# Optimization experiments

Measured on AMD Instinct MI355X. Metric: run time of the kernel, lower is better.

Reference implementation:

```python
import jax, jax.numpy as jnp
import numpy as np

B, S, D, MAX_LEN = 8, 2048, 512, 2048
NEG_INF = jnp.float32(-jnp.inf)


def setup_inputs() -> dict:
    key = jax.random.key(0)
    ks = jax.random.split(key, 10)
    s = 1.0 / np.sqrt(D)
    inp = {
        "x": jax.random.normal(ks[0], (B, S, D), dtype=jnp.float32),
        "pos_table": jax.random.normal(ks[1], (MAX_LEN, D), dtype=jnp.float32) * 0.02,
        "Wq": jax.random.normal(ks[2], (D, D), dtype=jnp.float32) * s,
        "bq": jnp.zeros((D,), dtype=jnp.float32),
        "Wk": jax.random.normal(ks[3], (D, D), dtype=jnp.float32) * s,
        "bk": jnp.zeros((D,), dtype=jnp.float32),
        "Wv": jax.random.normal(ks[4], (D, D), dtype=jnp.float32) * s,
        "bv": jnp.zeros((D,), dtype=jnp.float32),
        "Wd": jax.random.normal(ks[5], (D, D), dtype=jnp.float32) * s,
        "bd": jnp.zeros((D,), dtype=jnp.float32),
    }
    return inp


def reference(x, pos_table, Wq, bq, Wk, bk, Wv, bv, Wd, bd):
    # add learned positional embeddings (add_pos=True path): arange over seq dim
    x = x + pos_table[:x.shape[-2]]  # [B,S,D]
    # torch nn.Linear: y = x @ W.T + b
    q = jnp.einsum("bsd,ed->bse", x, Wq) + bq
    k = jnp.einsum("bsd,ed->bse", x, Wk) + bk
    v = jnp.einsum("bsd,ed->bse", x, Wv) + bv
    v = jnp.where(jnp.isnan(v), 0.0, v)  # nan_to_num(nan=0)
    scale = 1.0 / jnp.sqrt(jnp.float32(D))
    scores = jnp.einsum("bqd,bkd->bqk", q, k) * scale  # [B,S,S]
    scores = jnp.where(jnp.isnan(scores), NEG_INF, scores)  # nan_to_num(nan=-inf)
    attn = jax.nn.softmax(scores, axis=2)
    y = jnp.einsum("bqk,bkd->bqd", attn, v)
    return jnp.einsum("bsd,ed->bse", y, Wd) + bd
```

## Files before the change

### kernel.cpp

```cpp
#include <hip/hip_runtime.h>
#include <stdint.h>

typedef __bf16 bf16x8 __attribute__((ext_vector_type(8)));
typedef float f32x4 __attribute__((ext_vector_type(4)));

static constexpr float QK_SCALE = 0.044194173824159216f;

__device__ __forceinline__ uint16_t f2bf(float f) {
    uint32_t x = __builtin_bit_cast(uint32_t, f);
    x += 0x7FFFu + ((x >> 16) & 1u);
    return (uint16_t)(x >> 16);
}

__device__ __forceinline__ void cp16(const uint16_t* g, uint16_t* l) {
    __builtin_amdgcn_global_load_lds(
        (__attribute__((address_space(1))) void*)(uint16_t*)g,
        (__attribute__((address_space(3))) void*)l,
        16, 0, 0);
}

template <int MODE>
__global__ __launch_bounds__(256, 2) void gemm_nt(
    const uint16_t* __restrict__ A, const uint16_t* __restrict__ Bm,
    void* __restrict__ C0, void* __restrict__ C1, void* __restrict__ C2,
    const float* __restrict__ bias0, const float* __restrict__ bias1,
    const float* __restrict__ bias2,
    float scale, int K, int ldc, long bsA, long bsB, long bsC)
{
    __shared__ __align__(16) uint16_t SH[4][8192];

    const int t  = threadIdx.x;
    const int bn = blockIdx.x, bm = blockIdx.y, bz = blockIdx.z;
    const int wave = t >> 6, lane = t & 63;
    const int wm = (wave >> 1) * 64, wn = (wave & 1) * 64;
    const int lm = lane & 15, lq = lane >> 4;
    const int sw = lq ^ ((lm >> 1) & 3);

    const uint16_t* Ab = A  + (long)bz * bsA + (long)bm * 128 * K;
    const uint16_t* Bb = Bm + (long)bz * bsB + (long)bn * 128 * K;

    long goff[2]; int loff[2];
#pragma unroll
    for (int j = 0; j < 2; ++j) {
        const int s  = j * 256 + t;
        const int r  = s >> 2;
        const int cs = s & 3;
        const int cg = cs ^ ((r >> 1) & 3);
        goff[j] = (long)r * K + cg * 8;
        loff[j] = s * 8;
    }

    const int KI = K >> 5;

#pragma unroll
    for (int st = 0; st < 3; ++st)
#pragma unroll
        for (int j = 0; j < 2; ++j) {
            cp16(Ab + goff[j] + st * 32, SH[st] + loff[j]);
            cp16(Bb + goff[j] + st * 32, SH[st] + 4096 + loff[j]);
        }

    f32x4 acc[4][4] = {};

    for (int k = 0; k < KI; ++k) {
        asm volatile("s_waitcnt vmcnt(8) lgkmcnt(0)\n\ts_barrier" ::: "memory");

        int kp = k + 3; if (kp >= KI) kp -= KI;
        uint16_t* dst = SH[(k + 3) & 3];
        const long ko = (long)kp * 32;
#pragma unroll
        for (int j = 0; j < 2; ++j) {
            cp16(Ab + goff[j] + ko, dst + loff[j]);
            cp16(Bb + goff[j] + ko, dst + 4096 + loff[j]);
        }

        const uint16_t* buf = SH[k & 3];
        bf16x8 af[4], bfr[4];
#pragma unroll
        for (int i = 0; i < 4; ++i)
            af[i]  = *(const bf16x8*)&buf[((wm + i * 16 + lm) * 4 + sw) * 8];
#pragma unroll
        for (int i = 0; i < 4; ++i)
            bfr[i] = *(const bf16x8*)&buf[4096 + ((wn + i * 16 + lm) * 4 + sw) * 8];
#pragma unroll
        for (int i = 0; i < 4; ++i)
#pragma unroll
            for (int j = 0; j < 4; ++j)
                acc[i][j] = __builtin_amdgcn_mfma_f32_16x16x32_bf16(
                    bfr[i], af[j], acc[i][j], 0, 0, 0);
    }

    const int mb = bm * 128 + wm + lm;
    const int nb = bn * 128 + wn + lq * 4;
#pragma unroll
    for (int i = 0; i < 4; ++i) {
        const int n = nb + i * 16;
        if (MODE == 0) {
#pragma unroll
            for (int j = 0; j < 4; ++j) {
                const int m = mb + j * 16;
                const uint32_t lo = (uint32_t)f2bf(acc[i][j][0] * scale) |
                                    ((uint32_t)f2bf(acc[i][j][1] * scale) << 16);
                const uint32_t hi = (uint32_t)f2bf(acc[i][j][2] * scale) |
                                    ((uint32_t)f2bf(acc[i][j][3] * scale) << 16);
                *(uint2*)&((uint16_t*)C0)[(long)bz * bsC + (long)m * ldc + n] =
                    make_uint2(lo, hi);
            }
        } else if (MODE == 2) {
            const float4 b4 = *(const float4*)&bias0[n];
#pragma unroll
            for (int j = 0; j < 4; ++j) {
                const int m = mb + j * 16;
                *(float4*)&((float*)C0)[(long)m * ldc + n] = make_float4(
                    acc[i][j][0] + b4.x, acc[i][j][1] + b4.y,
                    acc[i][j][2] + b4.z, acc[i][j][3] + b4.w);
            }
        } else {
            const int sec = n >> 9, nn = n & 511;
            const float* bp = sec == 0 ? bias0 : (sec == 1 ? bias1 : bias2);
            const float4 b4 = *(const float4*)&bp[nn];
#pragma unroll
            for (int j = 0; j < 4; ++j) {
                const int m = mb + j * 16;
                if (sec < 2) {
                    uint16_t* Cq = (uint16_t*)(sec == 0 ? C0 : C1);
                    const uint32_t lo = (uint32_t)f2bf(acc[i][j][0] + b4.x) |
                                        ((uint32_t)f2bf(acc[i][j][1] + b4.y) << 16);
                    const uint32_t hi = (uint32_t)f2bf(acc[i][j][2] + b4.z) |
                                        ((uint32_t)f2bf(acc[i][j][3] + b4.w) << 16);
                    *(uint2*)&Cq[(long)m * 512 + nn] = make_uint2(lo, hi);
                } else {
                    const int bb = m >> 11, ss = m & 2047;
                    uint16_t* vt = (uint16_t*)C2 + ((long)bb * 512 + nn) * 2048 + ss;
                    vt[0]        = f2bf(acc[i][j][0] + b4.x);
                    vt[2048]     = f2bf(acc[i][j][1] + b4.y);
                    vt[2 * 2048] = f2bf(acc[i][j][2] + b4.z);
                    vt[3 * 2048] = f2bf(acc[i][j][3] + b4.w);
                }
            }
        }
    }
}

__global__ __launch_bounds__(256) void prep_x(const float* __restrict__ x,
                                              const float* __restrict__ pos,
                                              uint16_t* __restrict__ xb)
{
    const long i8 = ((long)blockIdx.x * 256 + threadIdx.x) * 8;
    const long p8 = i8 & ((1l << 20) - 1);
    const float4* xv = (const float4*)(x + i8);
    const float4* pv = (const float4*)(pos + p8);
    const float4 a0 = xv[0], a1 = xv[1];
    const float4 b0 = pv[0], b1 = pv[1];
    uint16_t o[8];
    o[0] = f2bf(a0.x + b0.x); o[1] = f2bf(a0.y + b0.y);
    o[2] = f2bf(a0.z + b0.z); o[3] = f2bf(a0.w + b0.w);
    o[4] = f2bf(a1.x + b1.x); o[5] = f2bf(a1.y + b1.y);
    o[6] = f2bf(a1.z + b1.z); o[7] = f2bf(a1.w + b1.w);
    *(uint4*)(xb + i8) = *(uint4*)o;
}

__global__ __launch_bounds__(256) void prep_w(
    const float* __restrict__ Wq, const float* __restrict__ Wk,
    const float* __restrict__ Wv, const float* __restrict__ Wd,
    uint16_t* __restrict__ wqkv, uint16_t* __restrict__ wd)
{
    const long f = ((long)blockIdx.x * 256 + threadIdx.x) * 8;
    const int  w = (int)(f >> 18);
    const long off = f & 262143;
    const float* src = (w == 0) ? Wq : (w == 1) ? Wk : (w == 2) ? Wv : Wd;
    uint16_t* dst = (w < 3) ? (wqkv + (long)w * 262144 + off) : (wd + off);
    const float4* s4 = (const float4*)(src + off);
    const float4 a = s4[0], b = s4[1];
    uint16_t o[8];
    o[0] = f2bf(a.x); o[1] = f2bf(a.y); o[2] = f2bf(a.z); o[3] = f2bf(a.w);
    o[4] = f2bf(b.x); o[5] = f2bf(b.y); o[6] = f2bf(b.z); o[7] = f2bf(b.w);
    *(uint4*)dst = *(uint4*)o;
}

__global__ __launch_bounds__(256) void softmax_rows(uint16_t* __restrict__ P)
{
    uint16_t* p = P + (long)blockIdx.x * 2048;
    const int t = threadIdx.x;
    const int lane = t & 63, wave = t >> 6;

    uint4 raw = *(const uint4*)(p + t * 8);
    uint32_t u[4] = {raw.x, raw.y, raw.z, raw.w};
    float x[8];
#pragma unroll
    for (int i = 0; i < 4; ++i) {
        x[2 * i]     = __builtin_bit_cast(float, u[i] << 16);
        x[2 * i + 1] = __builtin_bit_cast(float, u[i] & 0xFFFF0000u);
    }
    float mx = x[0];
#pragma unroll
    for (int i = 1; i < 8; ++i) mx = fmaxf(mx, x[i]);
#pragma unroll
    for (int off = 32; off; off >>= 1) mx = fmaxf(mx, __shfl_xor(mx, off));
    __shared__ float sm[4], ss[4];
    if (lane == 0) sm[wave] = mx;
    __syncthreads();
    mx = fmaxf(fmaxf(sm[0], sm[1]), fmaxf(sm[2], sm[3]));

    float sum = 0.f;
#pragma unroll
    for (int i = 0; i < 8; ++i) { x[i] = __expf(x[i] - mx); sum += x[i]; }
#pragma unroll
    for (int off = 32; off; off >>= 1) sum += __shfl_xor(sum, off);
    if (lane == 0) ss[wave] = sum;
    __syncthreads();
    const float inv = 1.f / (ss[0] + ss[1] + ss[2] + ss[3]);

#pragma unroll
    for (int i = 0; i < 4; ++i) {
        const uint32_t lo = f2bf(x[2 * i] * inv);
        const uint32_t hi = f2bf(x[2 * i + 1] * inv);
        u[i] = lo | (hi << 16);
    }
    *(uint4*)(p + t * 8) = make_uint4(u[0], u[1], u[2], u[3]);
}

extern "C" void kernel_launch(void* const* d_in, const int* in_sizes, int n_in,
                              void* d_out, int out_size, void* d_ws, size_t ws_size,
                              hipStream_t stream)
{
    const float* x   = (const float*)d_in[0];
    const float* pos = (const float*)d_in[1];
    const float* Wq  = (const float*)d_in[2];
    const float* bq  = (const float*)d_in[3];
    const float* Wk  = (const float*)d_in[4];
    const float* bk  = (const float*)d_in[5];
    const float* Wv  = (const float*)d_in[6];
    const float* bv  = (const float*)d_in[7];
    const float* Wd  = (const float*)d_in[8];
    const float* bd  = (const float*)d_in[9];
    float* out = (float*)d_out;

    char* ws = (char*)d_ws;
    uint16_t* xb   = (uint16_t*)(ws);
    uint16_t* wqkv = (uint16_t*)(ws + 16777216);
    uint16_t* wd   = (uint16_t*)(ws + 18350080);
    uint16_t* Qb   = (uint16_t*)(ws + 18874368);
    uint16_t* Kb   = (uint16_t*)(ws + 35651584);
    uint16_t* Vt   = (uint16_t*)(ws + 52428800);
    uint16_t* Pb   = (uint16_t*)(ws + 69206016);
    uint16_t* yb   = (uint16_t*)(ws + 136314880);

    prep_x<<<4096, 256, 0, stream>>>(x, pos, xb);
    prep_w<<<512, 256, 0, stream>>>(Wq, Wk, Wv, Wd, wqkv, wd);

    gemm_nt<3><<<dim3(12, 128, 1), 256, 0, stream>>>(
        xb, wqkv, Qb, Kb, Vt, bq, bk, bv, 1.0f, 512, 512, 0, 0, 0);

    gemm_nt<0><<<dim3(16, 16, 8), 256, 0, stream>>>(
        Qb, Kb, Pb, nullptr, nullptr, nullptr, nullptr, nullptr,
        QK_SCALE, 512, 2048, (long)2048 * 512, (long)2048 * 512,
        (long)2048 * 2048);

    softmax_rows<<<16384, 256, 0, stream>>>(Pb);

    gemm_nt<0><<<dim3(4, 16, 8), 256, 0, stream>>>(
        Pb, Vt, yb, nullptr, nullptr, nullptr, nullptr, nullptr,
        1.0f, 2048, 512, (long)2048 * 2048, (long)512 * 2048,
        (long)2048 * 512);

    gemm_nt<2><<<dim3(4, 128, 1), 256, 0, stream>>>(
        yb, wd, out, nullptr, nullptr, bd, nullptr, nullptr,
        1.0f, 512, 512, 0, 0, 0);
}
```

Before: 300.9 us.

## Remap GEMM block IDs into XCD-aware 4x4 supertiles for L2 reuse

Replaces the 3D grid with a 1D grid and decodes each block index so that blocks landing on the same XCD (id & 7) cover a 4x4 supertile of output tiles, sharing A and B panels in that XCD's L2. Each launch passes the supertile column count and the supertiles per batch. The tail prefetch now clamps to the last K slice instead of wrapping to the start, which changes the redundant loads into re-reads of recent data. The decode adds integer divides and assumes the grid sizes divide evenly into groups of 16 blocks per XCD.

Result: faster. 284.5 us (-5.5%).

```diff
diff --git a/kernel.cpp b/kernel.cpp
--- a/kernel.cpp
+++ b/kernel.cpp
@@ -25,12 +25,25 @@
     void* __restrict__ C0, void* __restrict__ C1, void* __restrict__ C2,
     const float* __restrict__ bias0, const float* __restrict__ bias1,
     const float* __restrict__ bias2,
-    float scale, int K, int ldc, long bsA, long bsB, long bsC)
+    float scale, int K, int ldc, long bsA, long bsB, long bsC,
+    int scols, int stPerBatch)
 {
     __shared__ __align__(16) uint16_t SH[4][8192];
 
+    const uint32_t id  = blockIdx.x;
+    const uint32_t xcd = id & 7u;
+    const uint32_t p   = id >> 3;
+    const uint32_t q   = p >> 4;
+    const uint32_t w   = p & 15u;
+    const uint32_t g   = q * 8u + xcd;
+    const uint32_t bz  = g / (uint32_t)stPerBatch;
+    const uint32_t gs  = g - bz * (uint32_t)stPerBatch;
+    const uint32_t sr  = gs / (uint32_t)scols;
+    const uint32_t sc  = gs - sr * (uint32_t)scols;
+    const int bm = (int)(sr * 4u + (w >> 2));
+    const int bn = (int)(sc * 4u + (w & 3u));
+
     const int t  = threadIdx.x;
-    const int bn = blockIdx.x, bm = blockIdx.y, bz = blockIdx.z;
     const int wave = t >> 6, lane = t & 63;
     const int wm = (wave >> 1) * 64, wn = (wave & 1) * 64;
     const int lm = lane & 15, lq = lane >> 4;
@@ -65,7 +78,7 @@
     for (int k = 0; k < KI; ++k) {
         asm volatile("s_waitcnt vmcnt(8) lgkmcnt(0)\n\ts_barrier" ::: "memory");
 
-        int kp = k + 3; if (kp >= KI) kp -= KI;
+        int kp = k + 3; if (kp >= KI) kp = KI - 1;
         uint16_t* dst = SH[(k + 3) & 3];
         const long ko = (long)kp * 32;
 #pragma unroll
@@ -249,22 +262,22 @@
     prep_x<<<4096, 256, 0, stream>>>(x, pos, xb);
     prep_w<<<512, 256, 0, stream>>>(Wq, Wk, Wv, Wd, wqkv, wd);
 
-    gemm_nt<3><<<dim3(12, 128, 1), 256, 0, stream>>>(
-        xb, wqkv, Qb, Kb, Vt, bq, bk, bv, 1.0f, 512, 512, 0, 0, 0);
-
-    gemm_nt<0><<<dim3(16, 16, 8), 256, 0, stream>>>(
+    gemm_nt<3><<<1536, 256, 0, stream>>>(
+        xb, wqkv, Qb, Kb, Vt, bq, bk, bv, 1.0f, 512, 512, 0, 0, 0, 3, 96);
+
+    gemm_nt<0><<<2048, 256, 0, stream>>>(
         Qb, Kb, Pb, nullptr, nullptr, nullptr, nullptr, nullptr,
         QK_SCALE, 512, 2048, (long)2048 * 512, (long)2048 * 512,
-        (long)2048 * 2048);
+        (long)2048 * 2048, 4, 16);
 
     softmax_rows<<<16384, 256, 0, stream>>>(Pb);
 
-    gemm_nt<0><<<dim3(4, 16, 8), 256, 0, stream>>>(
+    gemm_nt<0><<<512, 256, 0, stream>>>(
         Pb, Vt, yb, nullptr, nullptr, nullptr, nullptr, nullptr,
         1.0f, 2048, 512, (long)2048 * 2048, (long)512 * 2048,
-        (long)2048 * 512);
-
-    gemm_nt<2><<<dim3(4, 128, 1), 256, 0, stream>>>(
+        (long)2048 * 512, 1, 4);
+
+    gemm_nt<2><<<512, 256, 0, stream>>>(
         yb, wd, out, nullptr, nullptr, bd, nullptr, nullptr,
-        1.0f, 512, 512, 0, 0, 0);
-}
+        1.0f, 512, 512, 0, 0, 0, 1, 32);
+}
```
